# Performance work log

Measured on AMD Instinct MI355X. Metric: run time of the kernel, lower is better.

The kernel has to match this reference:

```python
import jax, jax.numpy as jnp
import numpy as np

N, V = 2048, 32000


def setup_inputs() -> dict:
    key = jax.random.key(0)
    k1, k2 = jax.random.split(key)
    logits = jax.random.normal(k1, (N, V), jnp.float32) * 4.0
    # pre-drawn Gumbel noise => categorical sample via argmax(logits + gumbel)
    u = jax.random.uniform(k2, (N, V), jnp.float32, minval=1e-6, maxval=1.0 - 1e-6)
    gumbel = -jnp.log(-jnp.log(u))
    return {
        "logits": logits,
        "gumbel": gumbel,
        "temperature": jnp.float32(0.7),
        "top_p": jnp.float32(0.95),
        "top_k": 50,
        "accept_threshold": jnp.float32(0.9),
    }


def reference(logits, gumbel, temperature, top_p, top_k, accept_threshold):
    neg_inf = jnp.finfo(logits.dtype).min
    x = logits / temperature  # temperature > 0 path

    # --- top_p_logits: sort desc, cumsum of softmax, shift-by-one keep-top mask ---
    order = jnp.argsort(-x, axis=-1)                       # [N, V] descending order
    sorted_x = jnp.take_along_axis(x, order, axis=-1)
    cum = jnp.cumsum(jax.nn.softmax(sorted_x, axis=-1), axis=-1)
    remove_sorted = cum > top_p
    # shift right by one, always keep top-1 token
    remove_sorted = jnp.concatenate(
        [jnp.zeros_like(remove_sorted[..., :1]), remove_sorted[..., :-1]], axis=-1)
    inv = jnp.argsort(order, axis=-1)                      # inverse permutation
    remove = jnp.take_along_axis(remove_sorted, inv, axis=-1)
    x = jnp.where(remove, neg_inf, x)

    # --- top_k_logits: mask everything below the k-th largest ---
    kth = jax.lax.top_k(x, top_k)[0][..., -1:]             # [N, 1]
    x = jnp.where(x < kth, neg_inf, x)

    # --- softmax + categorical sample (Gumbel-argmax) + confidence ---
    probs = jax.nn.softmax(x, axis=-1)                     # [N, V]
    x0 = jnp.argmax(x + gumbel, axis=-1)                   # [N] sampled tokens
    initial_confidence = jnp.take_along_axis(probs, x0[:, None], axis=-1)[:, 0]
    confidence = initial_confidence                        # default (no margin/neg_entropy)

    # --- accept loop: accept above threshold; if none, accept top-1 confidence ---
    high = initial_confidence > accept_threshold           # [N] bool
    any_high = jnp.any(high)
    fallback = jnp.zeros_like(high).at[jnp.argmax(confidence)].set(True)
    accepted = jnp.where(any_high, high, fallback)

    return confidence, x0, initial_confidence, accepted
```

## Files before the change

kernel.cpp:

```cpp
#include <hip/hip_runtime.h>
#include <math.h>
#include <float.h>

#define VOCAB    32000
#define NT       256
#define NWAVES   (NT / 64)
#define CAP      1024
#define KMAX     64
#define KREF     24.0f
#define THETA0   14.0f
#define LOG2E    1.4426950408889634f
#define THT      ((THETA0 - KREF) * LOG2E)
#define FBDELTA  (12.0f * LOG2E)
#define NCHUNK   (VOCAB / 4)

typedef float vf4 __attribute__((ext_vector_type(4)));


#define PROCESS(v, jj)                                                              \
    {                                                                               \
        float t0 = fmaf((v).x, a, b);                                               \
        float t1 = fmaf((v).y, a, b);                                               \
        float t2 = fmaf((v).z, a, b);                                               \
        float t3 = fmaf((v).w, a, b);                                               \
        sA += exp2f(t0);                                                            \
        sB += exp2f(t1);                                                            \
        sA += exp2f(t2);                                                            \
        sB += exp2f(t3);                                                            \
        tmax = fmaxf(tmax, fmaxf(fmaxf(t0, t1), fmaxf(t2, t3)));                    \
        int bi = (jj) * 4;                                                          \
        if (t0 > THT) { int p = atomicAdd(&s_cnt, 1); if (p < CAP) { s_val[p] = (v).x / T; s_idx[p] = bi;     } } \
        if (t1 > THT) { int p = atomicAdd(&s_cnt, 1); if (p < CAP) { s_val[p] = (v).y / T; s_idx[p] = bi + 1; } } \
        if (t2 > THT) { int p = atomicAdd(&s_cnt, 1); if (p < CAP) { s_val[p] = (v).z / T; s_idx[p] = bi + 2; } } \
        if (t3 > THT) { int p = atomicAdd(&s_cnt, 1); if (p < CAP) { s_val[p] = (v).w / T; s_idx[p] = bi + 3; } } \
    }

__global__ __launch_bounds__(NT, 8) void dream_row_kernel(
    const float* __restrict__ logits,
    const float* __restrict__ gumbel,
    const float* __restrict__ tempP,
    const float* __restrict__ toppP,
    const int*   __restrict__ topkP,
    float* __restrict__ out_conf,
    float* __restrict__ out_x0,
    float* __restrict__ out_iconf)
{
    const int row = blockIdx.x;
    const int tid = threadIdx.x;
    const int lane = tid & 63;
    const int wid  = tid >> 6;
    const size_t base = (size_t)row * VOCAB;
    const vf4* l4 = (const vf4*)(logits + base);
    const float T = tempP[0];
    const float a = (1.0f / T) * LOG2E;
    const float b = -(KREF * LOG2E);

    __shared__ float s_val[CAP];
    __shared__ int   s_idx[CAP];
    __shared__ int   s_cnt;
    __shared__ float wsum[NWAVES], wmax[NWAVES];
    __shared__ float sh_S, sh_m;
    __shared__ float so_val[KMAX];
    __shared__ int   so_idx[KMAX];
    __shared__ int   sh_nk;
    __shared__ float sh_skept;

    if (tid == 0) s_cnt = 0;
    __syncthreads();

    float sA = 0.0f, sB = 0.0f;
    float tmax = -FLT_MAX;
    int j0 = tid;

    #pragma unroll 1
    for (int kb = 0; kb < 3; ++kb) {
        vf4 r0 = __builtin_nontemporal_load(&l4[j0 + 0 * NT]);
        vf4 r1 = __builtin_nontemporal_load(&l4[j0 + 1 * NT]);
        vf4 r2 = __builtin_nontemporal_load(&l4[j0 + 2 * NT]);
        vf4 r3 = __builtin_nontemporal_load(&l4[j0 + 3 * NT]);
        vf4 r4 = __builtin_nontemporal_load(&l4[j0 + 4 * NT]);
        vf4 r5 = __builtin_nontemporal_load(&l4[j0 + 5 * NT]);
        vf4 r6 = __builtin_nontemporal_load(&l4[j0 + 6 * NT]);
        vf4 r7 = __builtin_nontemporal_load(&l4[j0 + 7 * NT]);
        PROCESS(r0, j0 + 0 * NT);
        PROCESS(r1, j0 + 1 * NT);
        PROCESS(r2, j0 + 2 * NT);
        PROCESS(r3, j0 + 3 * NT);
        PROCESS(r4, j0 + 4 * NT);
        PROCESS(r5, j0 + 5 * NT);
        PROCESS(r6, j0 + 6 * NT);
        PROCESS(r7, j0 + 7 * NT);
        j0 += 8 * NT;
    }
    {
        vf4 r0 = __builtin_nontemporal_load(&l4[j0 + 0 * NT]);
        vf4 r1 = __builtin_nontemporal_load(&l4[j0 + 1 * NT]);
        vf4 r2 = __builtin_nontemporal_load(&l4[j0 + 2 * NT]);
        vf4 r3 = __builtin_nontemporal_load(&l4[j0 + 3 * NT]);
        vf4 r4 = __builtin_nontemporal_load(&l4[j0 + 4 * NT]);
        vf4 r5 = __builtin_nontemporal_load(&l4[j0 + 5 * NT]);
        vf4 r6 = __builtin_nontemporal_load(&l4[j0 + 6 * NT]);
        PROCESS(r0, j0 + 0 * NT);
        PROCESS(r1, j0 + 1 * NT);
        PROCESS(r2, j0 + 2 * NT);
        PROCESS(r3, j0 + 3 * NT);
        PROCESS(r4, j0 + 4 * NT);
        PROCESS(r5, j0 + 5 * NT);
        PROCESS(r6, j0 + 6 * NT);
        j0 += 7 * NT;
    }
    if (j0 < NCHUNK) {
        vf4 v = __builtin_nontemporal_load(&l4[j0]);
        PROCESS(v, j0);
    }

    float s = sA + sB;
    float mx = tmax;
    #pragma unroll
    for (int o = 32; o > 0; o >>= 1) {
        s  += __shfl_down(s, o, 64);
        mx  = fmaxf(mx, __shfl_down(mx, o, 64));
    }
    if (lane == 0) { wsum[wid] = s; wmax[wid] = mx; }
    __syncthreads();
    if (tid == 0) {
        float St = 0.0f, Mt = -FLT_MAX;
        #pragma unroll
        for (int w = 0; w < NWAVES; ++w) { St += wsum[w]; Mt = fmaxf(Mt, wmax[w]); }
        sh_S = St; sh_m = Mt;
    }
    __syncthreads();
    const float S_K = sh_S;
    const float m_t = sh_m;
    int C = min(s_cnt, CAP);

    if (C < KMAX) {
        if (tid == 0) s_cnt = 0;
        __syncthreads();
        const float th2t = m_t - FBDELTA;
        for (int j = tid; j < NCHUNK; j += NT) {
            vf4 v = __builtin_nontemporal_load(&l4[j]);
            float t0 = fmaf(v.x, a, b);
            float t1 = fmaf(v.y, a, b);
            float t2 = fmaf(v.z, a, b);
            float t3 = fmaf(v.w, a, b);
            int bi = j * 4;
            if (t0 > th2t) { int p = atomicAdd(&s_cnt, 1); if (p < CAP) { s_val[p] = v.x / T; s_idx[p] = bi;     } }
            if (t1 > th2t) { int p = atomicAdd(&s_cnt, 1); if (p < CAP) { s_val[p] = v.y / T; s_idx[p] = bi + 1; } }
            if (t2 > th2t) { int p = atomicAdd(&s_cnt, 1); if (p < CAP) { s_val[p] = v.z / T; s_idx[p] = bi + 2; } }
            if (t3 > th2t) { int p = atomicAdd(&s_cnt, 1); if (p < CAP) { s_val[p] = v.w / T; s_idx[p] = bi + 3; } }
        }
        __syncthreads();
        C = min(s_cnt, CAP);
    }

    for (int c = tid; c < C; c += NT) {
        float vc = s_val[c]; int ic = s_idx[c];
        int r = 0;
        #pragma unroll 4
        for (int j = 0; j < C; ++j) {
            float vj = s_val[j];
            if (vj > vc || (vj == vc && s_idx[j] < ic)) r++;
        }
        if (r < KMAX) { so_val[r] = vc; so_idx[r] = ic; }
    }
    __syncthreads();

    if (tid == 0) {
        int k = topkP[0]; if (k > KMAX) k = KMAX; if (k < 1) k = 1;
        const float topp = toppP[0];
        const int lim = min(C, k);
        float cum = 0.0f;
        float skept = 0.0f;
        int nk = 0;
        for (int j = 0; j < lim; ++j) {
            if (cum > topp) break;
            float e = exp2f(fmaf(so_val[j], LOG2E, b));
            cum += e / S_K;
            skept += e;
            nk++;
        }
        sh_nk = nk;
        sh_skept = skept;
    }
    __syncthreads();
    const int nk = sh_nk;
    const float skept = sh_skept;

    if (wid == 0) {
        float bv = -FLT_MAX; int bi = 0x7FFFFFFF; float bx = 0.0f;
        if (lane < nk) {
            int gi = so_idx[lane];
            bx = so_val[lane];
            bv = bx + gumbel[base + gi];
            bi = gi;
        }
        #pragma unroll
        for (int o = 32; o > 0; o >>= 1) {
            float ov = __shfl_down(bv, o, 64);
            int   oi = __shfl_down(bi, o, 64);
            float ox = __shfl_down(bx, o, 64);
            if (ov > bv || (ov == bv && oi < bi)) { bv = ov; bi = oi; bx = ox; }
        }
        if (lane == 0) {
            float eb = exp2f(fmaf(bx, LOG2E, b));
            float confv = eb / skept;
            out_conf[row]  = confv;
            out_x0[row]    = (float)bi;
            out_iconf[row] = confv;
        }
    }
}

__global__ __launch_bounds__(NT) void accept_kernel(
    const float* __restrict__ conf,
    const float* __restrict__ thrP,
    float* __restrict__ acc_out,
    int N)
{
    __shared__ float rv[NT];
    __shared__ int   ri[NT];
    __shared__ int   ra[NT];
    const int tid = threadIdx.x;
    const float thr = thrP[0];

    float bv = -FLT_MAX; int bi = 0x7FFFFFFF; int any = 0;
    for (int i = tid; i < N; i += NT) {
        float v = conf[i];
        if (v > thr) any = 1;
        if (v > bv) { bv = v; bi = i; }
    }
    rv[tid] = bv; ri[tid] = bi; ra[tid] = any;
    __syncthreads();
    #pragma unroll
    for (int s = NT / 2; s > 0; s >>= 1) {
        if (tid < s) {
            float ov = rv[tid + s]; int oi = ri[tid + s];
            if (ov > rv[tid] || (ov == rv[tid] && oi < ri[tid])) {
                rv[tid] = ov; ri[tid] = oi;
            }
            ra[tid] |= ra[tid + s];
        }
        __syncthreads();
    }
    const int anyHigh = ra[0];
    const int amax = ri[0];
    for (int i = tid; i < N; i += NT) {
        float a;
        if (anyHigh) a = (conf[i] > thr) ? 1.0f : 0.0f;
        else         a = (i == amax) ? 1.0f : 0.0f;
        acc_out[i] = a;
    }
}

extern "C" void kernel_launch(void* const* d_in, const int* in_sizes, int n_in,
                              void* d_out, int out_size, void* d_ws, size_t ws_size,
                              hipStream_t stream)
{
    const float* logits = (const float*)d_in[0];
    const float* gumbel = (const float*)d_in[1];
    const float* tempP  = (const float*)d_in[2];
    const float* toppP  = (const float*)d_in[3];
    const int*   topkP  = (const int*)d_in[4];
    const float* thrP   = (const float*)d_in[5];
    float* out = (float*)d_out;
    const int N = in_sizes[0] / VOCAB;

    dream_row_kernel<<<N, NT, 0, stream>>>(
        logits, gumbel, tempP, toppP, topkP,
        out , out + N , out + 2 * N );

    accept_kernel<<<1, NT, 0, stream>>>(
        out, thrP, out + 3 * N , N);
}
```

Before: 507.6 us.

## Split per-row kernel into grid-wide wave-chunk sweep plus per-row finalize

Replaces the one-block-per-row kernel with a persistent grid-stride sweep kernel. In it each wave handles one 256-float chunk of some row, writes per-chunk partial sums and maxes to workspace, and appends candidates above a threshold to per-row global buffers using global atomics. A second per-row kernel merges the partials, ranks the candidates, and does the top-p/top-k and Gumbel selection. The aim is to spread the logits streaming evenly across the GPU and shorten per-block latency. In exchange it adds a memset, an extra launch, global atomics and workspace traffic, and the legacy path remains as a fallback when workspace is too small.

```diff
diff --git a/kernel.cpp b/kernel.cpp
--- a/kernel.cpp
+++ b/kernel.cpp
@@ -6,6 +6,7 @@
 #define NT       256
 #define NWAVES   (NT / 64)
 #define CAP      1024
+#define CAPG     512
 #define KMAX     64
 #define KREF     24.0f
 #define THETA0   14.0f
@@ -13,9 +14,211 @@
 #define THT      ((THETA0 - KREF) * LOG2E)
 #define FBDELTA  (12.0f * LOG2E)
 #define NCHUNK   (VOCAB / 4)
+#define WCPR     125
 
 typedef float vf4 __attribute__((ext_vector_type(4)));
 
+
+#define SWEEP(vv, wc, row, cir)                                                   \
+    {                                                                             \
+        float t0 = fmaf((vv).x, a, b);                                            \
+        float t1 = fmaf((vv).y, a, b);                                            \
+        float t2 = fmaf((vv).z, a, b);                                            \
+        float t3 = fmaf((vv).w, a, b);                                            \
+        float s  = (exp2f(t0) + exp2f(t2)) + (exp2f(t1) + exp2f(t3));             \
+        float mx = fmaxf(fmaxf(t0, t1), fmaxf(t2, t3));                           \
+        _Pragma("unroll")                                                         \
+        for (int o = 32; o > 0; o >>= 1) {                                        \
+            s  += __shfl_down(s, o, 64);                                          \
+            mx  = fmaxf(mx, __shfl_down(mx, o, 64));                              \
+        }                                                                         \
+        if (lane == 0) { psum[wc] = s; pmaxv[wc] = mx; }                          \
+        int bi = ((cir) * 64 + lane) * 4;                                         \
+        if (t0 > THT) { int p = atomicAdd(&gcnt[row], 1); if (p < CAPG) { gval[(size_t)(row)*CAPG + p] = (vv).x / T; gidx[(size_t)(row)*CAPG + p] = bi;     } } \
+        if (t1 > THT) { int p = atomicAdd(&gcnt[row], 1); if (p < CAPG) { gval[(size_t)(row)*CAPG + p] = (vv).y / T; gidx[(size_t)(row)*CAPG + p] = bi + 1; } } \
+        if (t2 > THT) { int p = atomicAdd(&gcnt[row], 1); if (p < CAPG) { gval[(size_t)(row)*CAPG + p] = (vv).z / T; gidx[(size_t)(row)*CAPG + p] = bi + 2; } } \
+        if (t3 > THT) { int p = atomicAdd(&gcnt[row], 1); if (p < CAPG) { gval[(size_t)(row)*CAPG + p] = (vv).w / T; gidx[(size_t)(row)*CAPG + p] = bi + 3; } } \
+    }
+
+__global__ __launch_bounds__(NT, 8) void sweep_kernel(
+    const float* __restrict__ logits,
+    const float* __restrict__ tempP,
+    int*   __restrict__ gcnt,
+    float* __restrict__ psum,
+    float* __restrict__ pmaxv,
+    float* __restrict__ gval,
+    int*   __restrict__ gidx,
+    int nRows)
+{
+    const int tid  = threadIdx.x;
+    const int lane = tid & 63;
+    const int wid  = tid >> 6;
+    const float T = tempP[0];
+    const float a = (1.0f / T) * LOG2E;
+    const float b = -(KREF * LOG2E);
+    const int totalWC = nRows * WCPR;
+    const int mainWC  = totalWC & ~3;
+    const int gw = blockIdx.x * NWAVES + wid;
+    const int nw = gridDim.x * NWAVES;
+
+    for (int wcb = gw * 4; wcb < mainWC; wcb += nw * 4) {
+        int row0 = (wcb + 0) / WCPR, cir0 = (wcb + 0) - row0 * WCPR;
+        int row1 = (wcb + 1) / WCPR, cir1 = (wcb + 1) - row1 * WCPR;
+        int row2 = (wcb + 2) / WCPR, cir2 = (wcb + 2) - row2 * WCPR;
+        int row3 = (wcb + 3) / WCPR, cir3 = (wcb + 3) - row3 * WCPR;
+        const vf4* p0 = (const vf4*)logits + ((size_t)row0 * NCHUNK + cir0 * 64 + lane);
+        const vf4* p1 = (const vf4*)logits + ((size_t)row1 * NCHUNK + cir1 * 64 + lane);
+        const vf4* p2 = (const vf4*)logits + ((size_t)row2 * NCHUNK + cir2 * 64 + lane);
+        const vf4* p3 = (const vf4*)logits + ((size_t)row3 * NCHUNK + cir3 * 64 + lane);
+        vf4 r0 = __builtin_nontemporal_load(p0);
+        vf4 r1 = __builtin_nontemporal_load(p1);
+        vf4 r2 = __builtin_nontemporal_load(p2);
+        vf4 r3 = __builtin_nontemporal_load(p3);
+        SWEEP(r0, wcb + 0, row0, cir0);
+        SWEEP(r1, wcb + 1, row1, cir1);
+        SWEEP(r2, wcb + 2, row2, cir2);
+        SWEEP(r3, wcb + 3, row3, cir3);
+    }
+    for (int wc = mainWC + gw; wc < totalWC; wc += nw) {
+        int row = wc / WCPR, cir = wc - row * WCPR;
+        const vf4* p = (const vf4*)logits + ((size_t)row * NCHUNK + cir * 64 + lane);
+        vf4 r = __builtin_nontemporal_load(p);
+        SWEEP(r, wc, row, cir);
+    }
+}
+
+__global__ __launch_bounds__(NT) void finalize_kernel(
+    const float* __restrict__ logits,
+    const float* __restrict__ gumbel,
+    const float* __restrict__ tempP,
+    const float* __restrict__ toppP,
+    const int*   __restrict__ topkP,
+    const int*   __restrict__ gcnt,
+    const float* __restrict__ psum,
+    const float* __restrict__ pmaxv,
+    const float* __restrict__ gval,
+    const int*   __restrict__ gidx,
+    float* __restrict__ out_conf,
+    float* __restrict__ out_x0,
+    float* __restrict__ out_iconf)
+{
+    const int row = blockIdx.x;
+    const int tid = threadIdx.x;
+    const int lane = tid & 63;
+    const int wid  = tid >> 6;
+    const size_t base = (size_t)row * VOCAB;
+    const float T = tempP[0];
+    const float a = (1.0f / T) * LOG2E;
+    const float b = -(KREF * LOG2E);
+
+    __shared__ float s_val[CAP];
+    __shared__ int   s_idx[CAP];
+    __shared__ int   s_cnt;
+    __shared__ float redS[WCPR], redM[WCPR];
+    __shared__ float sh_S, sh_m;
+    __shared__ float so_val[KMAX];
+    __shared__ int   so_idx[KMAX];
+    __shared__ int   sh_nk;
+    __shared__ float sh_skept;
+
+    if (tid < WCPR) {
+        redS[tid] = psum[(size_t)row * WCPR + tid];
+        redM[tid] = pmaxv[(size_t)row * WCPR + tid];
+    }
+    int cnt = gcnt[row];
+    int C = min(cnt, CAPG);
+    for (int c = tid; c < C; c += NT) {
+        s_val[c] = gval[(size_t)row * CAPG + c];
+        s_idx[c] = gidx[(size_t)row * CAPG + c];
+    }
+    __syncthreads();
+    if (tid == 0) {
+        float S = 0.0f, M = -FLT_MAX;
+        for (int i = 0; i < WCPR; ++i) { S += redS[i]; M = fmaxf(M, redM[i]); }
+        sh_S = S; sh_m = M;
+    }
+    __syncthreads();
+    const float S_K = sh_S;
+    const float m_t = sh_m;
+
+    if (C < KMAX) {
+        if (tid == 0) s_cnt = 0;
+        __syncthreads();
+        const float th2t = m_t - FBDELTA;
+        const vf4* l4 = (const vf4*)(logits + base);
+        for (int j = tid; j < NCHUNK; j += NT) {
+            vf4 v = __builtin_nontemporal_load(&l4[j]);
+            float t0 = fmaf(v.x, a, b);
+            float t1 = fmaf(v.y, a, b);
+            float t2 = fmaf(v.z, a, b);
+            float t3 = fmaf(v.w, a, b);
+            int bi = j * 4;
+            if (t0 > th2t) { int p = atomicAdd(&s_cnt, 1); if (p < CAP) { s_val[p] = v.x / T; s_idx[p] = bi;     } }
+            if (t1 > th2t) { int p = atomicAdd(&s_cnt, 1); if (p < CAP) { s_val[p] = v.y / T; s_idx[p] = bi + 1; } }
+            if (t2 > th2t) { int p = atomicAdd(&s_cnt, 1); if (p < CAP) { s_val[p] = v.z / T; s_idx[p] = bi + 2; } }
+            if (t3 > th2t) { int p = atomicAdd(&s_cnt, 1); if (p < CAP) { s_val[p] = v.w / T; s_idx[p] = bi + 3; } }
+        }
+        __syncthreads();
+        C = min(s_cnt, CAP);
+    }
+
+    for (int c = tid; c < C; c += NT) {
+        float vc = s_val[c]; int ic = s_idx[c];
+        int r = 0;
+        #pragma unroll 4
+        for (int j = 0; j < C; ++j) {
+            float vj = s_val[j];
+            if (vj > vc || (vj == vc && s_idx[j] < ic)) r++;
+        }
+        if (r < KMAX) { so_val[r] = vc; so_idx[r] = ic; }
+    }
+    __syncthreads();
+
+    if (tid == 0) {
+        int k = topkP[0]; if (k > KMAX) k = KMAX; if (k < 1) k = 1;
+        const float topp = toppP[0];
+        const int lim = min(C, k);
+        float cum = 0.0f;
+        float skept = 0.0f;
+        int nk = 0;
+        for (int j = 0; j < lim; ++j) {
+            if (cum > topp) break;
+            float e = exp2f(fmaf(so_val[j], LOG2E, b));
+            cum += e / S_K;
+            skept += e;
+            nk++;
+        }
+        sh_nk = nk;
+        sh_skept = skept;
+    }
+    __syncthreads();
+    const int nk = sh_nk;
+    const float skept = sh_skept;
+
+    if (wid == 0) {
+        float bv = -FLT_MAX; int bi = 0x7FFFFFFF; float bx = 0.0f;
+        if (lane < nk) {
+            int gi = so_idx[lane];
+            bx = so_val[lane];
+            bv = bx + gumbel[base + gi];
+            bi = gi;
+        }
+        #pragma unroll
+        for (int o = 32; o > 0; o >>= 1) {
+            float ov = __shfl_down(bv, o, 64);
+            int   oi = __shfl_down(bi, o, 64);
+            float ox = __shfl_down(bx, o, 64);
+            if (ov > bv || (ov == bv && oi < bi)) { bv = ov; bi = oi; bx = ox; }
+        }
+        if (lane == 0) {
+            float eb = exp2f(fmaf(bx, LOG2E, b));
+            float confv = eb / skept;
+            out_conf[row]  = confv;
+            out_x0[row]    = (float)bi;
+            out_iconf[row] = confv;
+        }
+    }
+}
 
 #define PROCESS(v, jj)                                                              \
     {                                                                               \
@@ -35,7 +238,7 @@
         if (t3 > THT) { int p = atomicAdd(&s_cnt, 1); if (p < CAP) { s_val[p] = (v).w / T; s_idx[p] = bi + 3; } } \
     }
 
-__global__ __launch_bounds__(NT, 8) void dream_row_kernel(
+__global__ __launch_bounds__(NT, 8) void dream_row_legacy(
     const float* __restrict__ logits,
     const float* __restrict__ gumbel,
     const float* __restrict__ tempP,
@@ -71,7 +274,6 @@
     float sA = 0.0f, sB = 0.0f;
     float tmax = -FLT_MAX;
     int j0 = tid;
-
     #pragma unroll 1
     for (int kb = 0; kb < 3; ++kb) {
         vf4 r0 = __builtin_nontemporal_load(&l4[j0 + 0 * NT]);
@@ -266,9 +468,34 @@
     float* out = (float*)d_out;
     const int N = in_sizes[0] / VOCAB;
 
-    dream_row_kernel<<<N, NT, 0, stream>>>(
-        logits, gumbel, tempP, toppP, topkP,
-        out , out + N , out + 2 * N );
+    auto al = [](size_t x) { return (x + 255) & ~(size_t)255; };
+    size_t gcnt_o = 0;
+    size_t psum_o = al(gcnt_o + (size_t)N * 4);
+    size_t pmax_o = al(psum_o + (size_t)N * WCPR * 4);
+    size_t gval_o = al(pmax_o + (size_t)N * WCPR * 4);
+    size_t gidx_o = al(gval_o + (size_t)N * CAPG * 4);
+    size_t need   = gidx_o + (size_t)N * CAPG * 4;
+
+    if (ws_size >= need) {
+        char* ws = (char*)d_ws;
+        int*   gcnt  = (int*)(ws + gcnt_o);
+        float* psum  = (float*)(ws + psum_o);
+        float* pmaxv = (float*)(ws + pmax_o);
+        float* gval  = (float*)(ws + gval_o);
+        int*   gidx  = (int*)(ws + gidx_o);
+
+        hipMemsetAsync(gcnt, 0, (size_t)N * 4, stream);
+        sweep_kernel<<<2048, NT, 0, stream>>>(
+            logits, tempP, gcnt, psum, pmaxv, gval, gidx, N);
+        finalize_kernel<<<N, NT, 0, stream>>>(
+            logits, gumbel, tempP, toppP, topkP,
+            gcnt, psum, pmaxv, gval, gidx,
+            out , out + N , out + 2 * N );
+    } else {
+        dream_row_legacy<<<N, NT, 0, stream>>>(
+            logits, gumbel, tempP, toppP, topkP,
+            out, out + N, out + 2 * N);
+    }
 
     accept_kernel<<<1, NT, 0, stream>>>(
         out, thrP, out + 3 * N , N);
```

Result: slower. 708.1 us (+39.5%).
